# Optimization experiments

Hardware: AMD Instinct MI355X
Metric: run time of the kernel (lower is better)

Reference implementation:

```python
import jax, jax.numpy as jnp
import numpy as np
from jax import lax

SEQ_LEN, BATCH, POSE, H, PRED_LEN = 32, 32768, 34, 16, 15


def setup_inputs() -> dict:
    key = jax.random.key(0)
    ks = jax.random.split(key, 22)
    w = lambda k, s: (jax.random.normal(k, s, jnp.float32) * 0.1)
    return {
        "obs_s": jax.random.normal(ks[0], (SEQ_LEN, BATCH, POSE), jnp.float32),
        "enc_Wih": w(ks[1], (4 * H, POSE)), "enc_Whh": w(ks[2], (4 * H, H)),
        "enc_bih": w(ks[3], (4 * H,)), "enc_bhh": w(ks[4], (4 * H,)),
        "dec_Wih": w(ks[5], (4 * H, POSE)), "dec_Whh": w(ks[6], (4 * H, H)),
        "dec_bih": w(ks[7], (4 * H,)), "dec_bhh": w(ks[8], (4 * H,)),
        "cr_Wih": w(ks[9], (4 * H, POSE)), "cr_Whh": w(ks[10], (4 * H, H)),
        "cr_bih": w(ks[11], (4 * H,)), "cr_bhh": w(ks[12], (4 * H,)),
        "fc_W": w(ks[13], (POSE, H)), "fc_b": w(ks[14], (POSE,)),
        "fcc_W": w(ks[15], (2, H)), "fcc_b": w(ks[16], (2,)),
        "mlp_W": w(ks[17], (H, H)), "mlp_b": w(ks[18], (H,)),
        "emb_W": w(ks[19], (POSE, 2)), "emb_b": w(ks[20], (POSE,)),
        "pred_len": PRED_LEN,
    }


def _cell(x, h, c, Wih, Whh, bih, bhh):
    # torch LSTM gate order: i, f, g, o
    gates = x @ Wih.T + bih + h @ Whh.T + bhh  # [B, 4H]
    i, f, g, o = jnp.split(gates, 4, axis=-1)
    c = jax.nn.sigmoid(f) * c + jax.nn.sigmoid(i) * jnp.tanh(g)
    h = jax.nn.sigmoid(o) * jnp.tanh(c)
    return h, c


def reference(obs_s, enc_Wih, enc_Whh, enc_bih, enc_bhh,
              dec_Wih, dec_Whh, dec_bih, dec_bhh,
              cr_Wih, cr_Whh, cr_bih, cr_bhh,
              fc_W, fc_b, fcc_W, fcc_b, mlp_W, mlp_b, emb_W, emb_b,
              pred_len):
    batch = obs_s.shape[1]
    h0 = jnp.zeros((batch, H), obs_s.dtype)
    c0 = jnp.zeros((batch, H), obs_s.dtype)

    def enc_step(carry, x):
        h, c = _cell(x, *carry, enc_Wih, enc_Whh, enc_bih, enc_bhh)
        return (h, c), None

    (h, c), _ = lax.scan(enc_step, (h0, c0), obs_s)

    hc = h @ mlp_W.T + mlp_b           # crossing hidden init from encoder h
    cc = jnp.zeros_like(hc)
    last_s = obs_s[-1]                 # [B, POSE]
    last_cr = obs_s[-1]

    def dec_step(carry, _):
        h, c, hc, cc, last_s, last_cr = carry
        hc, cc = _cell(last_cr, hc, cc, cr_Wih, cr_Whh, cr_bih, cr_bhh)
        curr_cr = jax.nn.softmax(hc @ fcc_W.T + fcc_b, axis=-1)   # [B, 2]
        next_cr = curr_cr @ emb_W.T + emb_b                        # [B, POSE]
        h, c = _cell(last_s, h, c, dec_Wih, dec_Whh, dec_bih, dec_bhh)
        curr_s = h @ fc_W.T + fc_b                                 # [B, POSE]
        return (h, c, hc, cc, curr_s, next_cr), (curr_s, curr_cr)

    _, (pred_s, pred_crossing) = lax.scan(
        dec_step, (h, c, hc, cc, last_s, last_cr), None, length=pred_len)
    return pred_s, pred_crossing
```

## Files before the change

kernel.cpp:

```cpp
#include <hip/hip_runtime.h>
#include <cstddef>

#define SEQLEN 32
#define BATCH  32768
#define POSE   34
#define PREDL  15
#define LOG2E  1.4426950408889634f
#define K2E    2.8853901817779268f

typedef __attribute__((ext_vector_type(8))) short short8;
typedef __attribute__((ext_vector_type(4))) float f32x4;
typedef union { short8 s8; unsigned u[4]; } pk8;

#define MF(a,b,c) __builtin_amdgcn_mfma_f32_16x16x32_bf16(a,b,c,0,0,0)
#define EXP2(x)  __builtin_amdgcn_exp2f(x)
#define RCP(x)   __builtin_amdgcn_rcpf(x)

__device__ __forceinline__ unsigned short f2bf(float f){ __bf16 b=(__bf16)f; return __builtin_bit_cast(unsigned short,b); }
__device__ __forceinline__ unsigned f22bf(float lo,float hi){ return (unsigned)f2bf(lo) | ((unsigned)f2bf(hi)<<16); }
__device__ __forceinline__ short8 zero8(){ pk8 r; r.u[0]=0;r.u[1]=0;r.u[2]=0;r.u[3]=0; return r.s8; }
__device__ __forceinline__ float scGT(int gt){ return (gt==2)?K2E:LOG2E; }

__device__ __forceinline__ short8 g8s(const float* __restrict__ p, float s){
    pk8 r;
    r.u[0]=f22bf(p[0]*s,p[1]*s); r.u[1]=f22bf(p[2]*s,p[3]*s);
    r.u[2]=f22bf(p[4]*s,p[5]*s); r.u[3]=f22bf(p[6]*s,p[7]*s);
    return r.s8;
}

__device__ __forceinline__ void pw4v(const f32x4 (&ac)[4], f32x4 &cs,
                                     unsigned &hp0, unsigned &hp1){
    f32x4 A,C,B,O;
#pragma unroll
    for(int j=0;j<4;++j){
        A[j]=EXP2(-ac[0][j]); C[j]=EXP2(-ac[1][j]);
        B[j]=EXP2( ac[2][j]); O[j]=EXP2(-ac[3][j]);
    }
    const f32x4 one={1.f,1.f,1.f,1.f};
    f32x4 u=one+A, w=one+C, v=B+one, Bm=B-one;
    f32x4 t1=u*v;
    f32x4 num=cs*t1+Bm*w;
    f32x4 den=t1*w;
    f32x4 rd_,E,rh;
#pragma unroll
    for(int j=0;j<4;++j) rd_[j]=RCP(den[j]);
    f32x4 cn=num*rd_;
    cs=cn;
#pragma unroll
    for(int j=0;j<4;++j) E[j]=EXP2(K2E*cn[j]);
    f32x4 hd=(one+O)*(E+one);
#pragma unroll
    for(int j=0;j<4;++j) rh[j]=RCP(hd[j]);
    f32x4 hv=(E-one)*rh;
    hp0=f22bf(hv[0],hv[1]); hp1=f22bf(hv[2],hv[3]);
}

extern "C" __global__ void lstm_prep(
    const float* __restrict__ dWih, const float* __restrict__ dWhh,
    const float* __restrict__ dbih, const float* __restrict__ dbhh,
    const float* __restrict__ cWih, const float* __restrict__ cWhh,
    const float* __restrict__ cbih, const float* __restrict__ cbhh,
    const float* __restrict__ fcW,  const float* __restrict__ fcb,
    const float* __restrict__ embW, const float* __restrict__ embb,
    float* __restrict__ wsBD, float* __restrict__ wsBC,
    unsigned short* __restrict__ wsDh, unsigned short* __restrict__ wsCh,
    unsigned short* __restrict__ wsCp)
{
    int idx = blockIdx.x*256 + threadIdx.x;
    if(idx < 1024){
        int R=idx>>4, k=idx&15;
        float s=scGT(R>>4);
        float vD=dWhh[R*16+k];
        for(int p=0;p<34;++p) vD=fmaf(dWih[R*34+p],fcW[p*16+k],vD);
        wsDh[idx]=f2bf(vD*s);
        wsCh[idx]=f2bf(cWhh[R*16+k]*s);
    }
    if(idx < 128){
        int R=idx>>1, k=idx&1;
        float s=scGT(R>>4);
        float v=0.f;
        for(int p=0;p<34;++p) v=fmaf(cWih[R*34+p],embW[2*p+k],v);
        wsCp[idx]=f2bf(v*s);
    }
    if(idx < 64){
        int R=idx;
        float s=scGT(R>>4);
        float vD=dbih[R]+dbhh[R], vC=cbih[R]+cbhh[R];
        for(int p=0;p<34;++p){ vD=fmaf(dWih[R*34+p],fcb[p],vD); vC=fmaf(cWih[R*34+p],embb[p],vC); }
        wsBD[idx]=vD*s; wsBC[idx]=vC*s;
    }
}

extern "C" __global__ void __launch_bounds__(256,2) lstm_w5(
    const float* __restrict__ obs_s,
    const float* __restrict__ eWih, const float* __restrict__ eWhh,
    const float* __restrict__ ebih, const float* __restrict__ ebhh,
    const float* __restrict__ dWih, const float* __restrict__ dWhh,
    const float* __restrict__ dbih, const float* __restrict__ dbhh,
    const float* __restrict__ cWih, const float* __restrict__ cWhh,
    const float* __restrict__ cbih, const float* __restrict__ cbhh,
    const float* __restrict__ fcW,  const float* __restrict__ fcb,
    const float* __restrict__ fccW, const float* __restrict__ fccb,
    const float* __restrict__ mlpW, const float* __restrict__ mlpb,
    const float* __restrict__ wsBD, const float* __restrict__ wsBC,
    const unsigned short* __restrict__ wsDh, const unsigned short* __restrict__ wsCh,
    const unsigned short* __restrict__ wsCp,
    float* __restrict__ out_s, float* __restrict__ out_cr)
{
    __shared__ unsigned xt4[4][4][320];

    const int tid=threadIdx.x;
    const int l=tid&63;
    const int wv=tid>>6;
    const int lo=l&15, g=l>>4;
    const int pb=blockIdx.x*64 + wv*16;
    unsigned* XT=&xt4[wv][0][0];

    unsigned pofs[5]; int wofs[5];
#pragma unroll
    for(int it=0; it<5; ++it){
        int i2=l+64*it;
        int r=i2/17, w=i2-r*17;
        pofs[it]=(unsigned)((pb+r)*17+w);
        wofs[it]=r*20+w;
    }

    short8 wEx[4], wEhT[4]; f32x4 biasE[4];
#pragma unroll
    for(int gt=0;gt<4;++gt){
        float s=scGT(gt);
        int R=gt*16+lo;
        wEx[gt]=g8s(&eWih[R*34+8*g], s);
        pk8 r2;
        r2.u[0]=f22bf(eWhh[R*16+4*g]*s,   eWhh[R*16+4*g+1]*s);
        r2.u[1]=f22bf(eWhh[R*16+4*g+2]*s, eWhh[R*16+4*g+3]*s);
        r2.u[2]=(g==0)? f22bf(eWih[R*34+32]*s, eWih[R*34+33]*s) : 0u;
        r2.u[3]=0u;
        wEhT[gt]=r2.s8;
        float4 ba=*(const float4*)&ebih[gt*16+4*g];
        float4 bb=*(const float4*)&ebhh[gt*16+4*g];
        biasE[gt]=f32x4{(ba.x+bb.x)*s,(ba.y+bb.y)*s,(ba.z+bb.z)*s,(ba.w+bb.w)*s};
    }

    f32x4 cS={0.f,0.f,0.f,0.f};
    unsigned hp0=0u, hp1=0u;

    float2 RA[4][5];
    auto ldblk=[&](float2 (&R)[4][5], int t0){
#pragma unroll
        for(int s=0;s<4;++s){
            const float2* base=(const float2*)obs_s + (size_t)(t0+s)*(BATCH*17);
#pragma unroll
            for(int it=0;it<5;++it)
                if(it<4 || l<16) R[s][it]=base[pofs[it]];
        }
    };
    auto wrblk=[&](const float2 (&R)[4][5]){
#pragma unroll
        for(int s=0;s<4;++s)
#pragma unroll
            for(int it=0;it<5;++it)
                if(it<4 || l<16) XT[s*320+wofs[it]]=f22bf(R[s][it].x,R[s][it].y);
    };

    short8 fbQ=zero8(); unsigned ftQ=0u;
    ldblk(RA,0);
#pragma unroll
    for(int kb=0;kb<8;++kb){
        wrblk(RA);
        if(kb+1<8) ldblk(RA,4*(kb+1));
        short8 bx[4]; unsigned tw[4];
#pragma unroll
        for(int s=0;s<4;++s){
            bx[s]=*(const short8*)&XT[s*320+lo*20+4*g];
            tw[s]=XT[s*320+lo*20+16];
        }
        f32x4 cx[4][4];
#pragma unroll
        for(int s=0;s<4;++s)
#pragma unroll
            for(int gt=0;gt<4;++gt)
                cx[s][gt]=MF(wEx[gt],bx[s],biasE[gt]);
        if(kb==7){ fbQ=bx[3]; ftQ=tw[3]; }
#pragma unroll
        for(int s=0;s<4;++s){
            pk8 bh; bh.u[0]=hp0; bh.u[1]=hp1; bh.u[2]=(g==0)?tw[s]:0u; bh.u[3]=0u;
            f32x4 acc[4];
#pragma unroll
            for(int gt=0;gt<4;++gt) acc[gt]=MF(wEhT[gt],bh.s8,cx[s][gt]);
            pw4v(acc,cS,hp0,hp1);
        }
    }

    short8 wDh[4], wCA[4]; f32x4 biasD[4], biasC[4];
#pragma unroll
    for(int gt=0;gt<4;++gt){
        int R=gt*16+lo;
        uint2 qd=*(const uint2*)&wsDh[R*16+4*g];
        pk8 rd; rd.u[0]=qd.x; rd.u[1]=qd.y; rd.u[2]=0u; rd.u[3]=0u;
        wDh[gt]=rd.s8;
        uint2 qc=*(const uint2*)&wsCh[R*16+4*g];
        pk8 rc; rc.u[0]=qc.x; rc.u[1]=qc.y;
        rc.u[2]=(g==0)? *(const unsigned*)&wsCp[R*2] : 0u; rc.u[3]=0u;
        wCA[gt]=rc.s8;
        biasD[gt]=*(const f32x4*)&wsBD[gt*16+4*g];
        biasC[gt]=*(const f32x4*)&wsBC[gt*16+4*g];
    }
    short8 wF[3]; f32x4 fcbF[3];
#pragma unroll
    for(int nt=0;nt<3;++nt){
        int np=nt*16+lo;
        if(np<POSE){
            pk8 r;
            r.u[0]=f22bf(fcW[np*16+4*g],   fcW[np*16+4*g+1]);
            r.u[1]=f22bf(fcW[np*16+4*g+2], fcW[np*16+4*g+3]);
            r.u[2]=0u; r.u[3]=0u;
            wF[nt]=r.s8;
        } else wF[nt]=zero8();
#pragma unroll
        for(int j=0;j<4;++j){
            int row=nt*16+4*g+j;
            fcbF[nt][j]=(row<POSE)? fcb[row] : 0.f;
        }
    }
    short8 wFC, wM; f32x4 fccC, mlpbF;
    if(lo<2){
        pk8 r;
        r.u[0]=f22bf(fccW[lo*16+4*g],   fccW[lo*16+4*g+1]);
        r.u[1]=f22bf(fccW[lo*16+4*g+2], fccW[lo*16+4*g+3]);
        r.u[2]=0u; r.u[3]=0u; wFC=r.s8;
    } else wFC=zero8();
    fccC=(g==0)? f32x4{fccb[0],fccb[1],0.f,0.f} : f32x4{0.f,0.f,0.f,0.f};
    {
        pk8 r;
        r.u[0]=f22bf(mlpW[lo*16+4*g],   mlpW[lo*16+4*g+1]);
        r.u[1]=f22bf(mlpW[lo*16+4*g+2], mlpW[lo*16+4*g+3]);
        r.u[2]=0u; r.u[3]=0u; wM=r.s8;
        mlpbF=*(const f32x4*)&mlpb[4*g];
    }

    unsigned hcp0,hcp1;
    {
        pk8 bh; bh.u[0]=hp0; bh.u[1]=hp1; bh.u[2]=0u; bh.u[3]=0u;
        f32x4 o=MF(wM,bh.s8,mlpbF);
        hcp0=f22bf(o[0],o[1]); hcp1=f22bf(o[2],o[3]);
    }
    f32x4 cC={0.f,0.f,0.f,0.f};
    unsigned pp=0u;

    auto dec_tail=[&](int s, const f32x4 (&aC)[4], const f32x4 (&aD)[4]){
        pw4v(aD,cS,hp0,hp1);
        pw4v(aC,cC,hcp0,hcp1);
        pk8 bhc; bhc.u[0]=hcp0; bhc.u[1]=hcp1; bhc.u[2]=0u; bhc.u[3]=0u;
        f32x4 zz=MF(wFC,bhc.s8,fccC);
        float z0=zz[0], z1=zz[1];
        float mx=fmaxf(z0,z1);
        float e0=EXP2(LOG2E*(z0-mx)), e1=EXP2(LOG2E*(z1-mx));
        float rs=RCP(e0+e1);
        float p0=e0*rs, p1=e1*rs;
        unsigned ppn=f22bf(p0,p1);
        if(g==0)
            ((float2*)out_cr)[(size_t)s*BATCH+pb+lo]=make_float2(p0,p1);
        pp=(unsigned)__shfl((int)ppn, lo, 64);
        pk8 bh; bh.u[0]=hp0; bh.u[1]=hp1; bh.u[2]=0u; bh.u[3]=0u;
        float* po = out_s + ((size_t)s*BATCH + pb + lo)*POSE;
        f32x4 o0=MF(wF[0],bh.s8,fcbF[0]);
        f32x4 o1=MF(wF[1],bh.s8,fcbF[1]);
        *(float2*)(po+4*g)     =make_float2(o0[0],o0[1]);
        *(float2*)(po+4*g+2)   =make_float2(o0[2],o0[3]);
        *(float2*)(po+16+4*g)  =make_float2(o1[0],o1[1]);
        *(float2*)(po+16+4*g+2)=make_float2(o1[2],o1[3]);
        f32x4 o2=MF(wF[2],bh.s8,fcbF[2]);
        if(g==0) *(float2*)(po+32)=make_float2(o2[0],o2[1]);
    };

    {
        f32x4 aC[4], aD[4];
#pragma unroll
        for(int gt=0;gt<4;++gt){
            float s=scGT(gt);
            int R=gt*16+lo;
            short8 a1=g8s(&cWih[R*34+8*g], s);
            pk8 a2;
            a2.u[0]=f22bf(cWhh[R*16+4*g]*s,   cWhh[R*16+4*g+1]*s);
            a2.u[1]=f22bf(cWhh[R*16+4*g+2]*s, cWhh[R*16+4*g+3]*s);
            a2.u[2]=(g==0)? f22bf(cWih[R*34+32]*s, cWih[R*34+33]*s) : 0u;
            a2.u[3]=0u;
            float4 ba=*(const float4*)&cbih[gt*16+4*g];
            float4 bb=*(const float4*)&cbhh[gt*16+4*g];
            f32x4 bc0={(ba.x+bb.x)*s,(ba.y+bb.y)*s,(ba.z+bb.z)*s,(ba.w+bb.w)*s};
            pk8 bhc; bhc.u[0]=hcp0; bhc.u[1]=hcp1; bhc.u[2]=(g==0)?ftQ:0u; bhc.u[3]=0u;
            f32x4 cx=MF(a1,fbQ,bc0);
            aC[gt]=MF(a2.s8,bhc.s8,cx);
            short8 d1=g8s(&dWih[R*34+8*g], s);
            pk8 d2;
            d2.u[0]=f22bf(dWhh[R*16+4*g]*s,   dWhh[R*16+4*g+1]*s);
            d2.u[1]=f22bf(dWhh[R*16+4*g+2]*s, dWhh[R*16+4*g+3]*s);
            d2.u[2]=(g==0)? f22bf(dWih[R*34+32]*s, dWih[R*34+33]*s) : 0u;
            d2.u[3]=0u;
            float4 da=*(const float4*)&dbih[gt*16+4*g];
            float4 db=*(const float4*)&dbhh[gt*16+4*g];
            f32x4 bd0={(da.x+db.x)*s,(da.y+db.y)*s,(da.z+db.z)*s,(da.w+db.w)*s};
            pk8 bhd; bhd.u[0]=hp0; bhd.u[1]=hp1; bhd.u[2]=(g==0)?ftQ:0u; bhd.u[3]=0u;
            f32x4 dx=MF(d1,fbQ,bd0);
            aD[gt]=MF(d2.s8,bhd.s8,dx);
        }
        dec_tail(0,aC,aD);
    }
    for(int s=1;s<PREDL;++s){
        pk8 bd; bd.u[0]=hp0; bd.u[1]=hp1; bd.u[2]=0u; bd.u[3]=0u;
        pk8 bc; bc.u[0]=hcp0; bc.u[1]=hcp1; bc.u[2]=(g==0)?pp:0u; bc.u[3]=0u;
        f32x4 aC[4], aD[4];
#pragma unroll
        for(int gt=0;gt<4;++gt) aD[gt]=MF(wDh[gt],bd.s8,biasD[gt]);
#pragma unroll
        for(int gt=0;gt<4;++gt) aC[gt]=MF(wCA[gt],bc.s8,biasC[gt]);
        dec_tail(s,aC,aD);
    }
}

extern "C" void kernel_launch(void* const* d_in, const int* in_sizes, int n_in,
                              void* d_out, int out_size, void* d_ws, size_t ws_size,
                              hipStream_t stream)
{
    const float* obs  = (const float*)d_in[0];
    const float* eWih = (const float*)d_in[1];
    const float* eWhh = (const float*)d_in[2];
    const float* ebih = (const float*)d_in[3];
    const float* ebhh = (const float*)d_in[4];
    const float* dWih = (const float*)d_in[5];
    const float* dWhh = (const float*)d_in[6];
    const float* dbih = (const float*)d_in[7];
    const float* dbhh = (const float*)d_in[8];
    const float* cWih = (const float*)d_in[9];
    const float* cWhh = (const float*)d_in[10];
    const float* cbih = (const float*)d_in[11];
    const float* cbhh = (const float*)d_in[12];
    const float* fcW  = (const float*)d_in[13];
    const float* fcb  = (const float*)d_in[14];
    const float* fccW = (const float*)d_in[15];
    const float* fccb = (const float*)d_in[16];
    const float* mlpW = (const float*)d_in[17];
    const float* mlpb = (const float*)d_in[18];
    const float* embW = (const float*)d_in[19];
    const float* embb = (const float*)d_in[20];

    float* out_s  = (float*)d_out;
    float* out_cr = out_s + (size_t)PREDL*BATCH*POSE;

    float* wsBD = (float*)d_ws;
    float* wsBC = wsBD + 64;
    unsigned short* wsDh = (unsigned short*)(wsBC+64);
    unsigned short* wsCh = wsDh + 1024;
    unsigned short* wsCp = wsCh + 1024;

    hipLaunchKernelGGL(lstm_prep, dim3(4), dim3(256), 0, stream,
                       dWih, dWhh, dbih, dbhh, cWih, cWhh, cbih, cbhh,
                       fcW, fcb, embW, embb, wsBD, wsBC, wsDh, wsCh, wsCp);
    hipLaunchKernelGGL(lstm_w5, dim3(BATCH/64), dim3(256), 0, stream,
                       obs, eWih, eWhh, ebih, ebhh, dWih, dWhh, dbih, dbhh,
                       cWih, cWhh, cbih, cbhh, fcW, fcb, fccW, fccb,
                       mlpW, mlpb, wsBD, wsBC, wsDh, wsCh, wsCp,
                       out_s, out_cr);
}
```

Baseline: 64.51 us.

## Stream encoder inputs via direct global-to-LDS loads with 6-slot ring buffer

Replaces the register-staged load/convert/LDS-write path for the encoder input sequence with global_load_lds direct copies into a per-wave 6-step ring buffer in LDS. Timesteps are consumed two at a time, with manual vmcnt waits and sched barriers so the next two steps' loads are in flight while the current ones compute. The bf16 conversion now happens after reading fp32 from LDS. The intent is to remove register pressure and VALU work from staging and to deepen the prefetch, at the cost of roughly doubled LDS use (fp32 instead of bf16), which may limit occupancy, and fragile hand-set waitcnt values.

```diff
diff --git a/kernel.cpp b/kernel.cpp
--- a/kernel.cpp
+++ b/kernel.cpp
@@ -27,6 +27,23 @@
     r.u[2]=f22bf(p[4]*s,p[5]*s); r.u[3]=f22bf(p[6]*s,p[7]*s);
     return r.s8;
 }
+
+__device__ __forceinline__ void gll4(const float* g, float* l){
+    __builtin_amdgcn_global_load_lds(
+        (const __attribute__((address_space(1))) unsigned*)g,
+        (__attribute__((address_space(3))) unsigned*)l, 4, 0, 0);
+}
+__device__ __forceinline__ unsigned ldsoff(const void* p){
+    return (unsigned)(unsigned long long)(const __attribute__((address_space(3))) void*)p;
+}
+__device__ __forceinline__ float2 ds_rd64(unsigned addr){
+    float2 r;
+    asm volatile("ds_read_b64 %0, %1" : "=v"(r) : "v"(addr));
+    return r;
+}
+#define WAIT_VM(N)  asm volatile("s_waitcnt vmcnt(" #N ")" ::: "memory")
+#define WAIT_LGKM() asm volatile("s_waitcnt lgkmcnt(0)" ::: "memory")
+#define SB0()       __builtin_amdgcn_sched_barrier(0)
 
 __device__ __forceinline__ void pw4v(const f32x4 (&ac)[4], f32x4 &cs,
                                      unsigned &hp0, unsigned &hp1){
@@ -91,7 +108,7 @@
     }
 }
 
-extern "C" __global__ void __launch_bounds__(256,2) lstm_w5(
+extern "C" __global__ void __launch_bounds__(256,2) lstm_wA(
     const float* __restrict__ obs_s,
     const float* __restrict__ eWih, const float* __restrict__ eWhh,
     const float* __restrict__ ebih, const float* __restrict__ ebhh,
@@ -107,23 +124,27 @@
     const unsigned short* __restrict__ wsCp,
     float* __restrict__ out_s, float* __restrict__ out_cr)
 {
-    __shared__ unsigned xt4[4][4][320];
+    __shared__ float xt6[4][6][544];
 
     const int tid=threadIdx.x;
     const int l=tid&63;
     const int wv=tid>>6;
     const int lo=l&15, g=l>>4;
     const int pb=blockIdx.x*64 + wv*16;
-    unsigned* XT=&xt4[wv][0][0];
-
-    unsigned pofs[5]; int wofs[5];
-#pragma unroll
-    for(int it=0; it<5; ++it){
-        int i2=l+64*it;
-        int r=i2/17, w=i2-r*17;
-        pofs[it]=(unsigned)((pb+r)*17+w);
-        wofs[it]=r*20+w;
-    }
+
+    auto issue_step=[&](int t,int slot){
+        const float* gb = obs_s + ((size_t)t*BATCH + pb)*34 + l;
+        float* lb = &xt6[wv][slot][0];
+#pragma unroll
+        for(int it=0; it<8; ++it) gll4(gb + 64*it, lb + 64*it);
+        if(l<32) gll4(gb + 512, lb + 512);
+    };
+#pragma unroll
+    for(int t=0;t<6;++t) issue_step(t,t);
+
+    const unsigned xbW = ldsoff(&xt6[wv][0][0]);
+    const unsigned xbG = xbW + (unsigned)(lo*136 + g*32);
+    const unsigned xbT = xbW + (unsigned)(lo*136 + 128);
 
     short8 wEx[4], wEhT[4]; f32x4 biasE[4];
 #pragma unroll
@@ -144,50 +165,48 @@
 
     f32x4 cS={0.f,0.f,0.f,0.f};
     unsigned hp0=0u, hp1=0u;
-
-    float2 RA[4][5];
-    auto ldblk=[&](float2 (&R)[4][5], int t0){
-#pragma unroll
-        for(int s=0;s<4;++s){
-            const float2* base=(const float2*)obs_s + (size_t)(t0+s)*(BATCH*17);
-#pragma unroll
-            for(int it=0;it<5;++it)
-                if(it<4 || l<16) R[s][it]=base[pofs[it]];
+    short8 fbQ=zero8(); unsigned ftQ=0u;
+
+#pragma unroll
+    for(int Tb=0; Tb<16; ++Tb){
+        const int T=2*Tb;
+        if(T<=26)      WAIT_VM(36);
+        else if(T==28) WAIT_VM(18);
+        else           WAIT_VM(0);
+        SB0();
+        const unsigned b0=xbG + (unsigned)((T  )%6)*2176u;
+        const unsigned b1=xbG + (unsigned)((T+1)%6)*2176u;
+        const unsigned t0=xbT + (unsigned)((T  )%6)*2176u;
+        const unsigned t1=xbT + (unsigned)((T+1)%6)*2176u;
+        float2 r0[4], r1[4], tl0, tl1;
+#pragma unroll
+        for(int q=0;q<4;++q){ r0[q]=ds_rd64(b0+8u*q); r1[q]=ds_rd64(b1+8u*q); }
+        tl0=ds_rd64(t0); tl1=ds_rd64(t1);
+        WAIT_LGKM();
+        SB0();
+        short8 bx[2]; unsigned tw2[2];
+        {
+            pk8 p0,p1;
+#pragma unroll
+            for(int q=0;q<4;++q){ p0.u[q]=f22bf(r0[q].x,r0[q].y); p1.u[q]=f22bf(r1[q].x,r1[q].y); }
+            bx[0]=p0.s8; bx[1]=p1.s8;
+            tw2[0]=f22bf(tl0.x,tl0.y); tw2[1]=f22bf(tl1.x,tl1.y);
         }
-    };
-    auto wrblk=[&](const float2 (&R)[4][5]){
-#pragma unroll
-        for(int s=0;s<4;++s)
-#pragma unroll
-            for(int it=0;it<5;++it)
-                if(it<4 || l<16) XT[s*320+wofs[it]]=f22bf(R[s][it].x,R[s][it].y);
-    };
-
-    short8 fbQ=zero8(); unsigned ftQ=0u;
-    ldblk(RA,0);
-#pragma unroll
-    for(int kb=0;kb<8;++kb){
-        wrblk(RA);
-        if(kb+1<8) ldblk(RA,4*(kb+1));
-        short8 bx[4]; unsigned tw[4];
-#pragma unroll
-        for(int s=0;s<4;++s){
-            bx[s]=*(const short8*)&XT[s*320+lo*20+4*g];
-            tw[s]=XT[s*320+lo*20+16];
-        }
-        f32x4 cx[4][4];
-#pragma unroll
-        for(int s=0;s<4;++s)
+        SB0();
+        if(T+6<SEQLEN){ issue_step(T+6,(T+6)%6); issue_step(T+7,(T+7)%6); }
+        f32x4 cx[2][4];
+#pragma unroll
+        for(int s2=0;s2<2;++s2)
 #pragma unroll
             for(int gt=0;gt<4;++gt)
-                cx[s][gt]=MF(wEx[gt],bx[s],biasE[gt]);
-        if(kb==7){ fbQ=bx[3]; ftQ=tw[3]; }
-#pragma unroll
-        for(int s=0;s<4;++s){
-            pk8 bh; bh.u[0]=hp0; bh.u[1]=hp1; bh.u[2]=(g==0)?tw[s]:0u; bh.u[3]=0u;
+                cx[s2][gt]=MF(wEx[gt],bx[s2],biasE[gt]);
+        if(T==30){ fbQ=bx[1]; ftQ=tw2[1]; }
+#pragma unroll
+        for(int s2=0;s2<2;++s2){
+            pk8 bh; bh.u[0]=hp0; bh.u[1]=hp1; bh.u[2]=(g==0)?tw2[s2]:0u; bh.u[3]=0u;
             f32x4 acc[4];
 #pragma unroll
-            for(int gt=0;gt<4;++gt) acc[gt]=MF(wEhT[gt],bh.s8,cx[s][gt]);
+            for(int gt=0;gt<4;++gt) acc[gt]=MF(wEhT[gt],bh.s8,cx[s2][gt]);
             pw4v(acc,cS,hp0,hp1);
         }
     }
@@ -357,7 +376,7 @@
     hipLaunchKernelGGL(lstm_prep, dim3(4), dim3(256), 0, stream,
                        dWih, dWhh, dbih, dbhh, cWih, cWhh, cbih, cbhh,
                        fcW, fcb, embW, embb, wsBD, wsBC, wsDh, wsCh, wsCp);
-    hipLaunchKernelGGL(lstm_w5, dim3(BATCH/64), dim3(256), 0, stream,
+    hipLaunchKernelGGL(lstm_wA, dim3(BATCH/64), dim3(256), 0, stream,
                        obs, eWih, eWhh, ebih, ebhh, dWih, dWhh, dbih, dbhh,
                        cWih, cWhh, cbih, cbhh, fcW, fcb, fccW, fccb,
                        mlpW, mlpb, wsBD, wsBC, wsDh, wsCh, wsCp,
```

New measurement: 65.80 us. +2.0%, slower.
